# Optimization experiments

Measured on AMD Instinct MI355X. Metric: run time of the kernel, lower is better.

## Reference

```python
import jax, jax.numpy as jnp
import numpy as np

K = 3  # kernel_size
STRIDE, PAD, DIL = 1, 1, 1


def conv2d(x, w, b):
    out = jax.lax.conv_general_dilated(
        x, w, (STRIDE, STRIDE), [(PAD, PAD), (PAD, PAD)],
        rhs_dilation=(DIL, DIL), dimension_numbers=('NCHW', 'OIHW', 'NCHW'))
    return out + b[None, :, None, None]


def bilinear_sample(x, sy, sx):
    """grid_sample(mode=bilinear, padding_mode=zeros, align_corners=True).
    x: (B,C,H,W); sy,sx: (B,K2,Ho,Wo) pixel coords. Returns (B,C,K2,Ho,Wo)."""
    B, C, H, W = x.shape
    y0 = jnp.floor(sy); x0 = jnp.floor(sx)
    y1 = y0 + 1.0;      x1 = x0 + 1.0
    wy1 = sy - y0; wy0 = 1.0 - wy1
    wx1 = sx - x0; wx0 = 1.0 - wx1
    x_flat = x.reshape(B, C, H * W)

    def gather(iy, ix):
        mask = ((iy >= 0) & (iy <= H - 1) & (ix >= 0) & (ix <= W - 1)).astype(x.dtype)
        iyc = jnp.clip(iy, 0, H - 1).astype(jnp.int32)
        ixc = jnp.clip(ix, 0, W - 1).astype(jnp.int32)
        idx = (iyc * W + ixc).reshape(B, 1, -1)
        v = jnp.take_along_axis(x_flat, idx, axis=2).reshape(B, C, *iy.shape[1:])
        return v * mask[:, None]

    return (gather(y0, x0) * (wy0 * wx0)[:, None]
            + gather(y0, x1) * (wy0 * wx1)[:, None]
            + gather(y1, x0) * (wy1 * wx0)[:, None]
            + gather(y1, x1) * (wy1 * wx1)[:, None])


def setup_inputs() -> dict:
    key = jax.random.key(0)
    ks = jax.random.split(key, 6)
    B, C, H, W = 4, 64, 128, 128
    O = 64
    x = jax.random.normal(ks[0], (B, C, H, W), jnp.float32)
    weight = jax.random.normal(ks[1], (O, C, K, K), jnp.float32) * (1.0 / (C * K * K) ** 0.5)
    bias = jax.random.normal(ks[2], (O,), jnp.float32) * 0.1
    offset_w = jax.random.normal(ks[3], (2 * K * K, C, K, K), jnp.float32) * 0.1 / (C * K * K) ** 0.5
    offset_b = jnp.zeros((2 * K * K,), jnp.float32)
    mod_w = jax.random.normal(ks[4], (K * K, C, K, K), jnp.float32) * (1.0 / (C * K * K) ** 0.5)
    mod_b = jnp.ones((K * K,), jnp.float32)
    return {"x": x, "weight": weight, "bias": bias,
            "offset_w": offset_w, "offset_b": offset_b,
            "mod_w": mod_w, "mod_b": mod_b}


def reference(x, weight, bias, offset_w, offset_b, mod_w, mod_b):
    B, C, H, W = x.shape
    O = weight.shape[0]
    K2 = K * K
    Ho = (H + 2 * PAD - DIL * (K - 1) - 1) // STRIDE + 1
    Wo = (W + 2 * PAD - DIL * (K - 1) - 1) // STRIDE + 1

    offsets = conv2d(x, offset_w, offset_b)                # (B, 2*K2, Ho, Wo)
    modul = jax.nn.sigmoid(conv2d(x, mod_w, mod_b))        # (B, K2, Ho, Wo)

    off = offsets.reshape(B, 2, K2, Ho, Wo)
    off_y, off_x = off[:, 0], off[:, 1]

    base_y, base_x = jnp.meshgrid(jnp.arange(Ho, dtype=jnp.float32),
                                  jnp.arange(Wo, dtype=jnp.float32), indexing='ij')
    base_y = base_y * STRIDE - PAD + (K // 2) * DIL
    base_x = base_x * STRIDE - PAD + (K // 2) * DIL
    koffs = jnp.arange(-(K // 2), K // 2 + 1, dtype=jnp.float32)
    ky, kx = jnp.meshgrid(koffs, koffs, indexing='ij')
    ky = ky.reshape(-1); kx = kx.reshape(-1)               # (K2,)

    sample_y = base_y[None, None] + ky[None, :, None, None] + off_y  # (B,K2,Ho,Wo)
    sample_x = base_x[None, None] + kx[None, :, None, None] + off_x
    # torch code normalizes to [-1,1] with align_corners=True; pixel coords are
    # recovered identically, so we sample directly at (sample_y, sample_x).

    sampled = bilinear_sample(x, sample_y, sample_x)       # (B,C,K2,Ho,Wo)

    w_flat = weight.reshape(O, C, K2)
    out = jnp.einsum('bckhw,ock->bohw', sampled, w_flat)   # groups=1

    mod_mean = jnp.mean(modul, axis=1, keepdims=True)      # (B,1,Ho,Wo)
    out = out * mod_mean + bias[None, :, None, None]
    return out
```

## Files before the change

kernel.cpp:

```cpp
#include <hip/hip_runtime.h>
#include <math.h>

#define K 3
#define K2 9
#define BB 4
#define C 64
#define H 128
#define W 128
#define O 64
#define HW (H*W)
#define Ho 128
#define Wo 128
#define TILE 64
#define TSTR 80

typedef _Float16 half4v __attribute__((ext_vector_type(4)));
typedef _Float16 half8v __attribute__((ext_vector_type(8)));
typedef float float4v __attribute__((ext_vector_type(4)));

__device__ __forceinline__ half8v bcast8(_Float16 w) {
    half8v v = {w, w, w, w, w, w, w, w};
    return v;
}

__global__ __launch_bounds__(256) void prep_all(
    const float* __restrict__ x,
    const float* __restrict__ weight,
    const float* __restrict__ offset_w,
    const float* __restrict__ mod_w,
    _Float16* __restrict__ xh,
    _Float16* __restrict__ wB,
    _Float16* __restrict__ wAB)
{
    int t = threadIdx.x;
    if (blockIdx.x < BB * H) {
        __shared__ _Float16 tile[W][68];
        int by = blockIdx.x;
        int y = by % H, b = by / H;
        int xq = t & 31, cr = t >> 5;
        #pragma unroll
        for (int g = 0; g < 8; g++) {
            int c = g * 8 + cr;
            float4v v = *(const float4v*)&x[(((size_t)b * C + c) * H + y) * W + xq * 4];
            tile[xq * 4 + 0][c] = (_Float16)v[0];
            tile[xq * 4 + 1][c] = (_Float16)v[1];
            tile[xq * 4 + 2][c] = (_Float16)v[2];
            tile[xq * 4 + 3][c] = (_Float16)v[3];
        }
        __syncthreads();
        int xp2 = t >> 1, hf = t & 1;
        const _Float16* src = &tile[xp2][hf * 32];
        _Float16* dst = xh + (((size_t)b * H + y) * W + xp2) * 64 + hf * 32;
        #pragma unroll
        for (int i = 0; i < 8; i++)
            *(half4v*)(dst + i * 4) = *(const half4v*)(src + i * 4);
    } else {
        int i = (blockIdx.x - BB * H) * 256 + t;
        if (i < K2 * 2 * 4 * 64 * 8) {
            int jj = i & 7;
            int lane = (i >> 3) & 63;
            int q4 = (i >> 9) & 3;
            int i2 = i >> 11;
            int tap = i2 >> 1, s = i2 & 1;
            int ch = s * 32 + ((lane >> 4) & 3) * 8 + jj;
            int o = q4 * 16 + (lane & 15);
            wB[i] = (_Float16)weight[(o * C + ch) * 9 + tap];
        }
        if (i < K2 * 2 * 2 * 64 * 8) {
            int jj = i & 7;
            int lane = (i >> 3) & 63;
            int jt = (i >> 9) & 1;
            int i2 = i >> 10;
            int tap = i2 >> 1, s = i2 & 1;
            int ch = s * 32 + ((lane >> 4) & 3) * 8 + jj;
            int n = jt * 16 + (lane & 15);
            float wv = 0.f;
            if (n < 27)
                wv = (n < 18) ? offset_w[(n * C + ch) * 9 + tap]
                              : mod_w[((n - 18) * C + ch) * 9 + tap];
            wAB[i] = (_Float16)wv;
        }
    }
}

__global__ __launch_bounds__(256) void fused_kernel(
    const _Float16* __restrict__ xh,
    const _Float16* __restrict__ wB,
    const _Float16* __restrict__ wAB,
    const float* __restrict__ bias,
    const float* __restrict__ offset_b,
    const float* __restrict__ mod_b,
    float* __restrict__ out)
{
    __shared__ _Float16 s_W[4][2][16][TSTR];
    __shared__ unsigned int s_ai[K2 * TILE];
    __shared__ half4v s_wgt[K2 * TILE];
    __shared__ float s_mm[TILE];
    float* s_res = (float*)&s_W[0][0][0][0];
    float* s_out = (float*)&s_W[0][0][0][0];

    int blk = blockIdx.x;
    int xcd = blk & 7, idx = blk >> 3;
    int b  = xcd >> 1;
    int h  = ((xcd & 1) << 6) | (idx >> 1);
    int wt = idx & 1;
    int t  = threadIdx.x;
    int q  = t >> 6;
    int lane = t & 63;
    int m16 = lane & 15;
    int quad = (lane >> 4) & 3;
    int w0 = wt * TILE;
    int px = lane;
    int p4 = lane >> 2;
    int sg = lane & 3;

    const _Float16* xb = xh + (size_t)b * HW * 64;

    float4v acc2[2];
    #pragma unroll
    for (int jt = 0; jt < 2; jt++) { float4v z = {0.f,0.f,0.f,0.f}; acc2[jt] = z; }

    {
        int y = h - 1;
        int xv = w0 + q * 16 + p4 - 1;
        float m = ((y >= 0) ? 1.f : 0.f) * ((xv >= 0) ? 1.f : 0.f);
        int yc = max(y, 0), xc = max(xv, 0);
        const _Float16* src = xb + ((size_t)(yc * W + xc)) * 64 + sg * 8;
        half8v vm = bcast8((_Float16)m);
        *(half8v*)&s_W[q][0][p4][sg * 8]      = *(const half8v*)src * vm;
        *(half8v*)&s_W[q][0][p4][32 + sg * 8] = *(const half8v*)(src + 32) * vm;
    }

    #pragma unroll 1
    for (int tap = 0; tap < K2; tap++) {
        half8v n0, n1; _Float16 nm;
        if (tap < 8) {
            int tp = tap + 1;
            int ki = tp / 3, kj = tp % 3;
            int y = h + ki - 1;
            int xv = w0 + q * 16 + p4 + kj - 1;
            nm = (_Float16)(((y >= 0 && y < H) ? 1.f : 0.f) *
                            ((xv >= 0 && xv < W) ? 1.f : 0.f));
            int yc = min(max(y, 0), H - 1), xc = min(max(xv, 0), W - 1);
            const _Float16* src = xb + ((size_t)(yc * W + xc)) * 64 + sg * 8;
            n0 = *(const half8v*)src;
            n1 = *(const half8v*)(src + 32);
        }
        #pragma unroll
        for (int s = 0; s < 2; s++) {
            half8v af = *(const half8v*)&s_W[q][tap & 1][m16][s * 32 + quad * 8];
            #pragma unroll
            for (int jt = 0; jt < 2; jt++) {
                int widx = (((tap * 2 + s) * 2 + jt) * 64 + lane) * 8;
                half8v bf = *(const half8v*)(wAB + widx);
                acc2[jt] = __builtin_amdgcn_mfma_f32_16x16x32_f16(af, bf, acc2[jt], 0, 0, 0);
            }
        }
        if (tap < 8) {
            half8v vm = bcast8(nm);
            *(half8v*)&s_W[q][(tap + 1) & 1][p4][sg * 8]      = n0 * vm;
            *(half8v*)&s_W[q][(tap + 1) & 1][p4][32 + sg * 8] = n1 * vm;
        }
    }

    __syncthreads();
    #pragma unroll
    for (int jt = 0; jt < 2; jt++) {
        int n = jt * 16 + m16;
        if (n < 27) {
            #pragma unroll
            for (int r = 0; r < 4; r++)
                s_res[n * 65 + q * 16 + quad * 4 + r] = acc2[jt][r];
        }
    }
    __syncthreads();

    #pragma unroll
    for (int ee = 0; ee < 3; ee++) {
        int e = t + ee * 256;
        if (e < K2 * TILE) {
            int k = e >> 6, p = e & 63;
            float offy = s_res[k * 65 + p] + offset_b[k];
            float offx = s_res[(9 + k) * 65 + p] + offset_b[9 + k];
            float sy = (float)(h + k / 3 - 1) + offy;
            float sx = (float)(w0 + p + k % 3 - 1) + offx;
            float fy = floorf(sy), fx = floorf(sx);
            int y0 = (int)fy, x0 = (int)fx;
            float wy1 = sy - fy, wx1 = sx - fx;
            int y0c = min(max(y0, 0), H - 1), y1c = min(max(y0 + 1, 0), H - 1);
            int x0c = min(max(x0, 0), W - 1), x1c = min(max(x0 + 1, 0), W - 1);
            s_ai[e] = (unsigned int)(y0c * W + x0c)
                    | ((unsigned int)(x1c - x0c) << 14)
                    | ((unsigned int)(y1c - y0c) << 15);
            float wg0 = (1.f - wy1) * ((y0 >= 0 && y0 < H) ? 1.f : 0.f);
            float wg1 = wy1 * ((y0 + 1 >= 0 && y0 + 1 < H) ? 1.f : 0.f);
            float wg2 = (1.f - wx1) * ((x0 >= 0 && x0 < W) ? 1.f : 0.f);
            float wg3 = wx1 * ((x0 + 1 >= 0 && x0 + 1 < W) ? 1.f : 0.f);
            half4v wp4;
            wp4[0] = (_Float16)(wg0 * wg2);
            wp4[1] = (_Float16)(wg0 * wg3);
            wp4[2] = (_Float16)(wg1 * wg2);
            wp4[3] = (_Float16)(wg1 * wg3);
            s_wgt[e] = wp4;
        }
    }
    if (t < TILE) {
        float sm = 0.f;
        #pragma unroll
        for (int m = 0; m < 9; m++) {
            float z = s_res[(18 + m) * 65 + t] + mod_b[m];
            sm += 1.f / (1.f + expf(-z));
        }
        s_mm[t] = sm * (1.f / 9.f);
    }
    __syncthreads();

    float4v acc[4];
    #pragma unroll
    for (int i = 0; i < 4; i++) { float4v z = {0.f,0.f,0.f,0.f}; acc[i] = z; }

    {
        int e = q * 16 + p4;
        unsigned int ai = s_ai[e];
        half4v wg = s_wgt[e];
        int a00 = ai & 0x3FFF;
        int dxo = ((ai >> 14) & 1) * 64;
        int dyo = ((ai >> 15) & 1) * (W * 64);
        const _Float16* base = xb + (size_t)a00 * 64 + sg * 8;
        half8v v0 = *(const half8v*)(base)             * bcast8(wg[0])
                  + *(const half8v*)(base + dxo)       * bcast8(wg[1])
                  + *(const half8v*)(base + dyo)       * bcast8(wg[2])
                  + *(const half8v*)(base + dyo + dxo) * bcast8(wg[3]);
        half8v v1 = *(const half8v*)(base + 32)             * bcast8(wg[0])
                  + *(const half8v*)(base + 32 + dxo)       * bcast8(wg[1])
                  + *(const half8v*)(base + 32 + dyo)       * bcast8(wg[2])
                  + *(const half8v*)(base + 32 + dyo + dxo) * bcast8(wg[3]);
        *(half8v*)&s_W[q][0][p4][sg * 8]      = v0;
        *(half8v*)&s_W[q][0][p4][32 + sg * 8] = v1;
    }

    #pragma unroll 1
    for (int tap = 0; tap < K2; tap++) {
        half8v rr[8]; half4v wgp;
        if (tap < 8) {
            int e = (tap + 1) * 64 + q * 16 + p4;
            unsigned int ai = s_ai[e];
            wgp = s_wgt[e];
            int a00 = ai & 0x3FFF;
            int dxo = ((ai >> 14) & 1) * 64;
            int dyo = ((ai >> 15) & 1) * (W * 64);
            const _Float16* base = xb + (size_t)a00 * 64 + sg * 8;
            rr[0] = *(const half8v*)(base);
            rr[1] = *(const half8v*)(base + dxo);
            rr[2] = *(const half8v*)(base + dyo);
            rr[3] = *(const half8v*)(base + dyo + dxo);
            rr[4] = *(const half8v*)(base + 32);
            rr[5] = *(const half8v*)(base + 32 + dxo);
            rr[6] = *(const half8v*)(base + 32 + dyo);
            rr[7] = *(const half8v*)(base + 32 + dyo + dxo);
        }
        #pragma unroll
        for (int s = 0; s < 2; s++) {
            half8v af = *(const half8v*)&s_W[q][tap & 1][m16][s * 32 + quad * 8];
            #pragma unroll
            for (int ot = 0; ot < 4; ot++) {
                int widx = (((tap * 2 + s) * 4 + ot) * 64 + lane) * 8;
                half8v bf = *(const half8v*)(wB + widx);
                acc[ot] = __builtin_amdgcn_mfma_f32_16x16x32_f16(af, bf, acc[ot], 0, 0, 0);
            }
        }
        if (tap < 8) {
            half8v v0 = rr[0] * bcast8(wgp[0]) + rr[1] * bcast8(wgp[1])
                      + rr[2] * bcast8(wgp[2]) + rr[3] * bcast8(wgp[3]);
            half8v v1 = rr[4] * bcast8(wgp[0]) + rr[5] * bcast8(wgp[1])
                      + rr[6] * bcast8(wgp[2]) + rr[7] * bcast8(wgp[3]);
            *(half8v*)&s_W[q][(tap + 1) & 1][p4][sg * 8]      = v0;
            *(half8v*)&s_W[q][(tap + 1) & 1][p4][32 + sg * 8] = v1;
        }
    }

    __syncthreads();
    #pragma unroll
    for (int ot = 0; ot < 4; ot++) {
        #pragma unroll
        for (int r = 0; r < 4; r++)
            s_out[(ot * 16 + m16) * 65 + q * 16 + quad * 4 + r] = acc[ot][r];
    }
    __syncthreads();
    {
        float mm = s_mm[px];
        #pragma unroll
        for (int jj = 0; jj < 16; jj++) {
            int o = q * 16 + jj;
            out[(((size_t)b * O + o) * Ho + h) * Wo + w0 + px] =
                s_out[o * 65 + px] * mm + bias[o];
        }
    }
}

extern "C" void kernel_launch(void* const* d_in, const int* in_sizes, int n_in,
                              void* d_out, int out_size, void* d_ws, size_t ws_size,
                              hipStream_t stream) {
    const float* x        = (const float*)d_in[0];
    const float* weight   = (const float*)d_in[1];
    const float* bias     = (const float*)d_in[2];
    const float* offset_w = (const float*)d_in[3];
    const float* offset_b = (const float*)d_in[4];
    const float* mod_w    = (const float*)d_in[5];
    const float* mod_b    = (const float*)d_in[6];
    float* out = (float*)d_out;

    _Float16* wB  = (_Float16*)d_ws;
    _Float16* wAB = wB + 36864;
    _Float16* xh  = wAB + 18432;

    prep_all<<<BB * H + 144, 256, 0, stream>>>(
        x, weight, offset_w, mod_w, xh, wB, wAB);

    int nblk = BB * Ho * (Wo / TILE);
    fused_kernel<<<nblk, 256, 0, stream>>>(
        xh, wB, wAB, bias, offset_b, mod_b, out);
}
```

Measured before the change: 114.0 us.

## Feed MFMA B operand directly from registers, drop LDS staging of sampled tiles

The MFMA operands are swapped so each lane loads or bilinearly interpolates its own pixel's channels straight into the B-fragment registers, with weights taken as the A operand. This removes the double-buffered shared-memory staging of the im2col tile, and the shared-memory transpose before the output store, since accumulators now map directly to output pixels. It cuts LDS traffic and barriers but drops the explicit software prefetch of gathers in favour of a partial unroll. The output store now writes 16 contiguous floats per row segment instead of 64.

Result: slower. 135.6 us (+19.0%).

```diff
diff --git a/kernel.cpp b/kernel.cpp
--- a/kernel.cpp
+++ b/kernel.cpp
@@ -12,7 +12,6 @@
 #define Ho 128
 #define Wo 128
 #define TILE 64
-#define TSTR 80
 
 typedef _Float16 half4v __attribute__((ext_vector_type(4)));
 typedef _Float16 half8v __attribute__((ext_vector_type(8)));
@@ -92,12 +91,10 @@
     const float* __restrict__ mod_b,
     float* __restrict__ out)
 {
-    __shared__ _Float16 s_W[4][2][16][TSTR];
     __shared__ unsigned int s_ai[K2 * TILE];
     __shared__ half4v s_wgt[K2 * TILE];
+    __shared__ float s_res[27 * 65];
     __shared__ float s_mm[TILE];
-    float* s_res = (float*)&s_W[0][0][0][0];
-    float* s_out = (float*)&s_W[0][0][0][0];
 
     int blk = blockIdx.x;
     int xcd = blk & 7, idx = blk >> 3;
@@ -110,9 +107,8 @@
     int m16 = lane & 15;
     int quad = (lane >> 4) & 3;
     int w0 = wt * TILE;
-    int px = lane;
-    int p4 = lane >> 2;
-    int sg = lane & 3;
+    int pxg = q * 16 + m16;
+    int chq = quad * 8;
 
     const _Float16* xb = xh + (size_t)b * HW * 64;
 
@@ -120,57 +116,32 @@
     #pragma unroll
     for (int jt = 0; jt < 2; jt++) { float4v z = {0.f,0.f,0.f,0.f}; acc2[jt] = z; }
 
-    {
-        int y = h - 1;
-        int xv = w0 + q * 16 + p4 - 1;
-        float m = ((y >= 0) ? 1.f : 0.f) * ((xv >= 0) ? 1.f : 0.f);
-        int yc = max(y, 0), xc = max(xv, 0);
-        const _Float16* src = xb + ((size_t)(yc * W + xc)) * 64 + sg * 8;
-        half8v vm = bcast8((_Float16)m);
-        *(half8v*)&s_W[q][0][p4][sg * 8]      = *(const half8v*)src * vm;
-        *(half8v*)&s_W[q][0][p4][32 + sg * 8] = *(const half8v*)(src + 32) * vm;
-    }
-
-    #pragma unroll 1
+    #pragma unroll 3
     for (int tap = 0; tap < K2; tap++) {
-        half8v n0, n1; _Float16 nm;
-        if (tap < 8) {
-            int tp = tap + 1;
-            int ki = tp / 3, kj = tp % 3;
-            int y = h + ki - 1;
-            int xv = w0 + q * 16 + p4 + kj - 1;
-            nm = (_Float16)(((y >= 0 && y < H) ? 1.f : 0.f) *
-                            ((xv >= 0 && xv < W) ? 1.f : 0.f));
-            int yc = min(max(y, 0), H - 1), xc = min(max(xv, 0), W - 1);
-            const _Float16* src = xb + ((size_t)(yc * W + xc)) * 64 + sg * 8;
-            n0 = *(const half8v*)src;
-            n1 = *(const half8v*)(src + 32);
-        }
-        #pragma unroll
-        for (int s = 0; s < 2; s++) {
-            half8v af = *(const half8v*)&s_W[q][tap & 1][m16][s * 32 + quad * 8];
-            #pragma unroll
-            for (int jt = 0; jt < 2; jt++) {
-                int widx = (((tap * 2 + s) * 2 + jt) * 64 + lane) * 8;
-                half8v bf = *(const half8v*)(wAB + widx);
-                acc2[jt] = __builtin_amdgcn_mfma_f32_16x16x32_f16(af, bf, acc2[jt], 0, 0, 0);
-            }
-        }
-        if (tap < 8) {
-            half8v vm = bcast8(nm);
-            *(half8v*)&s_W[q][(tap + 1) & 1][p4][sg * 8]      = n0 * vm;
-            *(half8v*)&s_W[q][(tap + 1) & 1][p4][32 + sg * 8] = n1 * vm;
-        }
-    }
-
-    __syncthreads();
+        int ki = tap / 3, kj = tap % 3;
+        int y = h + ki - 1;
+        int xv = w0 + pxg + kj - 1;
+        _Float16 m = (_Float16)(((y >= 0 && y < H) ? 1.f : 0.f) *
+                                ((xv >= 0 && xv < W) ? 1.f : 0.f));
+        int yc = min(max(y, 0), H - 1), xc = min(max(xv, 0), W - 1);
+        const _Float16* src = xb + ((size_t)(yc * W + xc)) * 64 + chq;
+        half8v vm = bcast8(m);
+        half8v b0 = *(const half8v*)src * vm;
+        half8v b1 = *(const half8v*)(src + 32) * vm;
+        #pragma unroll
+        for (int jt = 0; jt < 2; jt++) {
+            half8v a0 = *(const half8v*)(wAB + (((tap * 2 + 0) * 2 + jt) * 64 + lane) * 8);
+            half8v a1 = *(const half8v*)(wAB + (((tap * 2 + 1) * 2 + jt) * 64 + lane) * 8);
+            acc2[jt] = __builtin_amdgcn_mfma_f32_16x16x32_f16(a0, b0, acc2[jt], 0, 0, 0);
+            acc2[jt] = __builtin_amdgcn_mfma_f32_16x16x32_f16(a1, b1, acc2[jt], 0, 0, 0);
+        }
+    }
     #pragma unroll
     for (int jt = 0; jt < 2; jt++) {
-        int n = jt * 16 + m16;
-        if (n < 27) {
-            #pragma unroll
-            for (int r = 0; r < 4; r++)
-                s_res[n * 65 + q * 16 + quad * 4 + r] = acc2[jt][r];
+        #pragma unroll
+        for (int r = 0; r < 4; r++) {
+            int n = jt * 16 + quad * 4 + r;
+            if (n < 27) s_res[n * 65 + pxg] = acc2[jt][r];
         }
     }
     __syncthreads();
@@ -219,81 +190,45 @@
     #pragma unroll
     for (int i = 0; i < 4; i++) { float4v z = {0.f,0.f,0.f,0.f}; acc[i] = z; }
 
-    {
-        int e = q * 16 + p4;
+    #pragma unroll 3
+    for (int tap = 0; tap < K2; tap++) {
+        int e = tap * 64 + pxg;
         unsigned int ai = s_ai[e];
         half4v wg = s_wgt[e];
         int a00 = ai & 0x3FFF;
         int dxo = ((ai >> 14) & 1) * 64;
         int dyo = ((ai >> 15) & 1) * (W * 64);
-        const _Float16* base = xb + (size_t)a00 * 64 + sg * 8;
-        half8v v0 = *(const half8v*)(base)             * bcast8(wg[0])
-                  + *(const half8v*)(base + dxo)       * bcast8(wg[1])
-                  + *(const half8v*)(base + dyo)       * bcast8(wg[2])
-                  + *(const half8v*)(base + dyo + dxo) * bcast8(wg[3]);
-        half8v v1 = *(const half8v*)(base + 32)             * bcast8(wg[0])
-                  + *(const half8v*)(base + 32 + dxo)       * bcast8(wg[1])
-                  + *(const half8v*)(base + 32 + dyo)       * bcast8(wg[2])
-                  + *(const half8v*)(base + 32 + dyo + dxo) * bcast8(wg[3]);
-        *(half8v*)&s_W[q][0][p4][sg * 8]      = v0;
-        *(half8v*)&s_W[q][0][p4][32 + sg * 8] = v1;
-    }
-
-    #pragma unroll 1
-    for (int tap = 0; tap < K2; tap++) {
-        half8v rr[8]; half4v wgp;
-        if (tap < 8) {
-            int e = (tap + 1) * 64 + q * 16 + p4;
-            unsigned int ai = s_ai[e];
-            wgp = s_wgt[e];
-            int a00 = ai & 0x3FFF;
-            int dxo = ((ai >> 14) & 1) * 64;
-            int dyo = ((ai >> 15) & 1) * (W * 64);
-            const _Float16* base = xb + (size_t)a00 * 64 + sg * 8;
-            rr[0] = *(const half8v*)(base);
-            rr[1] = *(const half8v*)(base + dxo);
-            rr[2] = *(const half8v*)(base + dyo);
-            rr[3] = *(const half8v*)(base + dyo + dxo);
-            rr[4] = *(const half8v*)(base + 32);
-            rr[5] = *(const half8v*)(base + 32 + dxo);
-            rr[6] = *(const half8v*)(base + 32 + dyo);
-            rr[7] = *(const half8v*)(base + 32 + dyo + dxo);
-        }
-        #pragma unroll
-        for (int s = 0; s < 2; s++) {
-            half8v af = *(const half8v*)&s_W[q][tap & 1][m16][s * 32 + quad * 8];
+        const _Float16* base = xb + (size_t)a00 * 64 + chq;
+        half8v vw0 = bcast8(wg[0]), vw1 = bcast8(wg[1]);
+        half8v vw2 = bcast8(wg[2]), vw3 = bcast8(wg[3]);
+        half8v b0 = *(const half8v*)(base)             * vw0
+                  + *(const half8v*)(base + dxo)       * vw1
+                  + *(const half8v*)(base + dyo)       * vw2
+                  + *(const half8v*)(base + dyo + dxo) * vw3;
+        half8v b1 = *(const half8v*)(base + 32)             * vw0
+                  + *(const half8v*)(base + 32 + dxo)       * vw1
+                  + *(const half8v*)(base + 32 + dyo)       * vw2
+                  + *(const half8v*)(base + 32 + dyo + dxo) * vw3;
+        #pragma unroll
+        for (int ot = 0; ot < 4; ot++) {
+            half8v a0 = *(const half8v*)(wB + (((tap * 2 + 0) * 4 + ot) * 64 + lane) * 8);
+            half8v a1 = *(const half8v*)(wB + (((tap * 2 + 1) * 4 + ot) * 64 + lane) * 8);
+            acc[ot] = __builtin_amdgcn_mfma_f32_16x16x32_f16(a0, b0, acc[ot], 0, 0, 0);
+            acc[ot] = __builtin_amdgcn_mfma_f32_16x16x32_f16(a1, b1, acc[ot], 0, 0, 0);
+        }
+    }
+
+    {
+        float mm = s_mm[pxg];
+        #pragma unroll
+        for (int ot = 0; ot < 4; ot++) {
+            float4v bv = *(const float4v*)&bias[ot * 16 + quad * 4];
             #pragma unroll
-            for (int ot = 0; ot < 4; ot++) {
-                int widx = (((tap * 2 + s) * 4 + ot) * 64 + lane) * 8;
-                half8v bf = *(const half8v*)(wB + widx);
-                acc[ot] = __builtin_amdgcn_mfma_f32_16x16x32_f16(af, bf, acc[ot], 0, 0, 0);
+            for (int r = 0; r < 4; r++) {
+                int o = ot * 16 + quad * 4 + r;
+                out[(((size_t)b * O + o) * Ho + h) * Wo + w0 + pxg] =
+                    acc[ot][r] * mm + bv[r];
             }
-        }
-        if (tap < 8) {
-            half8v v0 = rr[0] * bcast8(wgp[0]) + rr[1] * bcast8(wgp[1])
-                      + rr[2] * bcast8(wgp[2]) + rr[3] * bcast8(wgp[3]);
-            half8v v1 = rr[4] * bcast8(wgp[0]) + rr[5] * bcast8(wgp[1])
-                      + rr[6] * bcast8(wgp[2]) + rr[7] * bcast8(wgp[3]);
-            *(half8v*)&s_W[q][(tap + 1) & 1][p4][sg * 8]      = v0;
-            *(half8v*)&s_W[q][(tap + 1) & 1][p4][32 + sg * 8] = v1;
-        }
-    }
-
-    __syncthreads();
-    #pragma unroll
-    for (int ot = 0; ot < 4; ot++) {
-        #pragma unroll
-        for (int r = 0; r < 4; r++)
-            s_out[(ot * 16 + m16) * 65 + q * 16 + quad * 4 + r] = acc[ot][r];
-    }
-    __syncthreads();
-    {
-        float mm = s_mm[px];
-        #pragma unroll
-        for (int jj = 0; jj < 16; jj++) {
-            int o = q * 16 + jj;
-            out[(((size_t)b * O + o) * Ho + h) * Wo + w0 + px] =
-                s_out[o * 65 + px] * mm + bias[o];
         }
     }
 }
```
